# Kernel optimization log

Measured on AMD Instinct MI355X. Metric: run time of the kernel, lower is better.

Reference implementation:

```python
import jax, jax.numpy as jnp
import numpy as np

N = 100000
E = 1600000
D_IN = 50
D_H = 128
D_OUT = 128
EPS = 1e-5


def setup_inputs() -> dict:
    key = jax.random.key(0)
    ks = jax.random.split(key, 24)
    def w(k, shape, fan_in):
        return jax.random.normal(k, shape, jnp.float32) / np.sqrt(fan_in)
    inp = {
        'x': jax.random.normal(ks[0], (N, D_IN), jnp.float32),
        'edge_src': jax.random.randint(ks[1], (E,), 0, N, jnp.int32),
        'edge_dst': jax.random.randint(ks[2], (E,), 0, N, jnp.int32),
        # SAGEConv 1: D_IN -> D_H
        'Wl1': w(ks[3], (D_IN, D_H), D_IN), 'Wr1': w(ks[4], (D_IN, D_H), D_IN), 'b1': jnp.zeros((D_H,), jnp.float32),
        # SAGEConv 2: D_H -> D_H
        'Wl2': w(ks[5], (D_H, D_H), D_H), 'Wr2': w(ks[6], (D_H, D_H), D_H), 'b2': jnp.zeros((D_H,), jnp.float32),
        # SAGEConv 3: D_H -> D_OUT
        'Wl3': w(ks[7], (D_H, D_OUT), D_H), 'Wr3': w(ks[8], (D_H, D_OUT), D_H), 'b3': jnp.zeros((D_OUT,), jnp.float32),
        # skip linears (no bias)
        'Ws1': w(ks[9], (D_IN, D_H), D_IN), 'Ws2': w(ks[10], (D_IN, D_H), D_IN),
        # LayerNorm affine
        'lnw1': jnp.ones((D_H,), jnp.float32), 'lnb1': jnp.zeros((D_H,), jnp.float32),
        'lnw2': jnp.ones((D_H,), jnp.float32), 'lnb2': jnp.zeros((D_H,), jnp.float32),
        'lnw3': jnp.ones((D_OUT,), jnp.float32), 'lnb3': jnp.zeros((D_OUT,), jnp.float32),
        # PReLU scalar slopes (PyG init 0.25)
        'a1': jnp.float32(0.25), 'a2': jnp.float32(0.25), 'a3': jnp.float32(0.25),
    }
    return inp


def _sage(x, src, dst, Wl, Wr, b):
    # mean aggregation of source features at destinations, then linear + root
    msg = x[src]                                              # [E, d]
    agg = jax.ops.segment_sum(msg, dst, num_segments=N)       # [N, d]
    cnt = jax.ops.segment_sum(jnp.ones((src.shape[0],), x.dtype), dst, num_segments=N)
    mean = agg / jnp.maximum(cnt, 1.0)[:, None]
    return mean @ Wl + x @ Wr + b


def _graph_ln(x, w, b):
    # PyG LayerNorm mode='graph', batch=None: normalize over all nodes+channels
    xc = x - jnp.mean(x)
    std = jnp.sqrt(jnp.mean(xc * xc))
    return (xc / (std + EPS)) * w + b


def _prelu(x, a):
    return jnp.where(x >= 0, x, a * x)


def reference(x, edge_src, edge_dst, Wl1, Wr1, b1, Wl2, Wr2, b2, Wl3, Wr3, b3,
              Ws1, Ws2, lnw1, lnb1, lnw2, lnb2, lnw3, lnb3, a1, a2, a3):
    h1 = _sage(x, edge_src, edge_dst, Wl1, Wr1, b1)
    h1 = _prelu(_graph_ln(h1, lnw1, lnb1), a1)
    h2 = _sage(h1 + x @ Ws1, edge_src, edge_dst, Wl2, Wr2, b2)
    h2 = _prelu(_graph_ln(h2, lnw2, lnb2), a2)
    ret = _sage(h1 + h2 + x @ Ws2, edge_src, edge_dst, Wl3, Wr3, b3)
    ret = _prelu(_graph_ln(ret, lnw3, lnb3), a3)
    return ret
```

## Files before the change

### kernel.cpp

```cpp
#include <hip/hip_runtime.h>

#define D_IN 50
#define LN_EPS 1e-5f
#define BSH 8
#define MAXB 512
#define NSLOT 64

typedef __bf16 bf16_t;
typedef bf16_t bf16x8 __attribute__((ext_vector_type(8)));
typedef float f32x4_t __attribute__((ext_vector_type(4)));
typedef float f32x2_t __attribute__((ext_vector_type(2)));

#define STRIDE_ST 136

#define ACCP(r, A)                                                            \
    {                                                                         \
        A[0] += (f32x2_t){__uint_as_float((r).x << 16),                       \
                          __uint_as_float((r).x & 0xffff0000u)};              \
        A[1] += (f32x2_t){__uint_as_float((r).y << 16),                       \
                          __uint_as_float((r).y & 0xffff0000u)};              \
        A[2] += (f32x2_t){__uint_as_float((r).z << 16),                       \
                          __uint_as_float((r).z & 0xffff0000u)};              \
        A[3] += (f32x2_t){__uint_as_float((r).w << 16),                       \
                          __uint_as_float((r).w & 0xffff0000u)};              \
    }

__global__ void bucket_hist_k(const int* __restrict__ dst, int* __restrict__ bcnt,
                              double* __restrict__ lnacc, int e, int nb) {
    __shared__ int lh[MAXB];
    int t = threadIdx.x;
    if (blockIdx.x == 0 && t < 3 * NSLOT) {
        lnacc[t * 8] = 0.0;
        lnacc[t * 8 + 1] = 0.0;
    }
    for (int i = t; i < nb; i += 256) lh[i] = 0;
    __syncthreads();
    for (int i = blockIdx.x * 256 + t; i < e; i += gridDim.x * 256)
        atomicAdd(&lh[dst[i] >> BSH], 1);
    __syncthreads();
    for (int i = t; i < nb; i += 256) {
        int c = lh[i];
        if (c) atomicAdd(&bcnt[i * 16], c);
    }
}

__global__ void bscan_k(const int* __restrict__ bcnt, int* __restrict__ boff,
                        int* __restrict__ bpos, int nb, int e) {
    __shared__ int l[MAXB];
    int t = threadIdx.x;
    l[t] = (t < nb) ? bcnt[t * 16] : 0;
    __syncthreads();
    for (int off = 1; off < MAXB; off <<= 1) {
        int v = (t >= off) ? l[t - off] : 0;
        __syncthreads();
        l[t] += v;
        __syncthreads();
    }
    int excl = (t > 0) ? l[t - 1] : 0;
    if (t < nb) { boff[t] = excl; bpos[t * 16] = excl; }
    if (t == 0) boff[nb] = e;
}

__global__ void scatter_k(const int* __restrict__ src, const int* __restrict__ dst,
                          int* __restrict__ bpos, unsigned* __restrict__ pool,
                          int e, int nb) {
    __shared__ int lh[MAXB];
    __shared__ int lcur[MAXB];
    int t = threadIdx.x;
    for (int i = t; i < nb; i += 256) lh[i] = 0;
    __syncthreads();
    int chunk = (e + gridDim.x - 1) / gridDim.x;
    int s = blockIdx.x * chunk;
    int en = min(e, s + chunk);
    for (int i = s + t; i < en; i += 256)
        atomicAdd(&lh[dst[i] >> BSH], 1);
    __syncthreads();
    for (int i = t; i < nb; i += 256) {
        int c = lh[i];
        lcur[i] = c ? atomicAdd(&bpos[i * 16], c) : 0;
    }
    __syncthreads();
    for (int i = s + t; i < en; i += 256) {
        int d = dst[i];
        int p = atomicAdd(&lcur[d >> BSH], 1);
        pool[p] = (unsigned)src[i] | ((unsigned)(d & 255) << 17);
    }
}

__global__ void nhist_cfill_k(const unsigned* __restrict__ pool, const int* __restrict__ boff,
                              int* __restrict__ rp, int* __restrict__ col, int n) {
    __shared__ int lc[256];
    __shared__ int ls[256];
    __shared__ int lpos[256];
    int b = blockIdx.x, t = threadIdx.x;
    lc[t] = 0;
    __syncthreads();
    int s = boff[b], e = boff[b + 1];
    for (int i = s + t; i < e; i += 256) atomicAdd(&lc[pool[i] >> 17], 1);
    __syncthreads();
    int v = lc[t];
    ls[t] = v;
    __syncthreads();
    for (int off = 1; off < 256; off <<= 1) {
        int x = (t >= off) ? ls[t - off] : 0;
        __syncthreads();
        ls[t] += x;
        __syncthreads();
    }
    int excl = ls[t] - v;
    int nd = (b << BSH) + t;
    if (nd < n) rp[nd] = s + excl;
    if (nd == n - 1) rp[n] = e;
    lpos[t] = s + excl;
    __syncthreads();
    for (int i = s + t; i < e; i += 256) {
        unsigned pk = pool[i];
        int slot = atomicAdd(&lpos[pk >> 17], 1);
        col[slot] = (int)(pk & 0x1FFFFu);
    }
}

struct ConvDesc { const float* w; bf16_t* o; int kin; int kpad; };
struct ConvArgs { ConvDesc d[8]; };

__global__ void conv_w_k(ConvArgs args) {
    ConvDesc d = args.d[blockIdx.y];
    int i = blockIdx.x * 256 + threadIdx.x;
    int tot = 128 * d.kpad;
    if (i >= tot) return;
    int n = i / d.kpad, k = i - n * d.kpad;
    float v = (k < d.kin) ? d.w[(size_t)k * 128 + n] : 0.f;
    d.o[i] = (bf16_t)v;
}

__global__ void conv_x_k(const float* __restrict__ x, bf16_t* __restrict__ xb, int n) {
    int i = blockIdx.x * 256 + threadIdx.x;
    if (i >= n * 64) return;
    int node = i >> 6, k = i & 63;
    xb[i] = (k < D_IN) ? (bf16_t)x[node * D_IN + k] : (bf16_t)0.f;
}

__global__ void agg_bf64_k(const bf16_t* __restrict__ feat, const int* __restrict__ rp,
                           const int* __restrict__ col, bf16_t* __restrict__ mean, int n) {
    int wid = (blockIdx.x * blockDim.x + threadIdx.x) >> 6;
    int lane = threadIdx.x & 63;
    if (wid >= n) return;
    int start = rp[wid], end = rp[wid + 1];
    int lc = lane & 7;
    int g = lane >> 3;
    f32x2_t accA[4], accB[4];
#pragma unroll
    for (int k = 0; k < 4; k++) { accA[k] = (f32x2_t){0.f, 0.f}; accB[k] = (f32x2_t){0.f, 0.f}; }
    int e = start + g;
    if (e + 8 < end) {
        int i0 = col[e], i1 = col[e + 8];
        for (; e + 24 < end; e += 16) {
            uint4 r0 = *(const uint4*)(feat + (size_t)i0 * 64 + lc * 8);
            uint4 r1 = *(const uint4*)(feat + (size_t)i1 * 64 + lc * 8);
            i0 = col[e + 16];
            i1 = col[e + 24];
            ACCP(r0, accA);
            ACCP(r1, accB);
        }
        uint4 r0 = *(const uint4*)(feat + (size_t)i0 * 64 + lc * 8);
        uint4 r1 = *(const uint4*)(feat + (size_t)i1 * 64 + lc * 8);
        ACCP(r0, accA);
        ACCP(r1, accB);
        e += 16;
    }
    for (; e < end; e += 8) {
        uint4 r0 = *(const uint4*)(feat + (size_t)col[e] * 64 + lc * 8);
        ACCP(r0, accA);
    }
#pragma unroll
    for (int k = 0; k < 4; k++) accA[k] += accB[k];
    float aL[4], aH[4];
#pragma unroll
    for (int k = 0; k < 4; k++) { aL[k] = accA[k].x; aH[k] = accA[k].y; }
#pragma unroll
    for (int off = 8; off < 64; off <<= 1) {
#pragma unroll
        for (int k = 0; k < 4; k++) {
            aL[k] += __shfl_xor(aL[k], off);
            aH[k] += __shfl_xor(aH[k], off);
        }
    }
    int c = end - start;
    float invc = 1.f / (float)(c > 0 ? c : 1);
    if (lane < 8) {
        bf16x8 o;
#pragma unroll
        for (int k = 0; k < 4; k++) {
            o[2 * k] = (bf16_t)(aL[k] * invc);
            o[2 * k + 1] = (bf16_t)(aH[k] * invc);
        }
        *(bf16x8*)(mean + (size_t)wid * 64 + lc * 8) = o;
    }
}

__global__ void agg_bf128_k(const bf16_t* __restrict__ feat, const int* __restrict__ rp,
                            const int* __restrict__ col, bf16_t* __restrict__ mean, int n) {
    int wid = (blockIdx.x * blockDim.x + threadIdx.x) >> 6;
    int lane = threadIdx.x & 63;
    if (wid >= n) return;
    int start = rp[wid], end = rp[wid + 1];
    int lc = lane & 15;
    int g = lane >> 4;
    const uint* fp = (const uint*)feat + lc * 4;
    f32x2_t accA[4], accB[4];
#pragma unroll
    for (int k = 0; k < 4; k++) { accA[k] = (f32x2_t){0.f, 0.f}; accB[k] = (f32x2_t){0.f, 0.f}; }
    int e = start + g;
    int ng = (e < end) ? (((end - 1 - e) >> 2) + 1) : 0;
    int it = 0;
    for (; it + 4 <= ng; it += 4, e += 16) {
        int a = col[e], b = col[e + 4], c = col[e + 8], d = col[e + 12];
        uint4 r0 = *(const uint4*)(fp + (size_t)a * 64);
        uint4 r1 = *(const uint4*)(fp + (size_t)b * 64);
        uint4 r2 = *(const uint4*)(fp + (size_t)c * 64);
        uint4 r3 = *(const uint4*)(fp + (size_t)d * 64);
        ACCP(r0, accA);
        ACCP(r1, accB);
        ACCP(r2, accA);
        ACCP(r3, accB);
    }
    int rem = ng - it;
    if (rem > 0) {
        int a = col[e];
        int b = (rem > 1) ? col[e + 4] : a;
        int c = (rem > 2) ? col[e + 8] : b;
        uint4 r0 = *(const uint4*)(fp + (size_t)a * 64);
        uint4 r1 = *(const uint4*)(fp + (size_t)b * 64);
        uint4 r2 = *(const uint4*)(fp + (size_t)c * 64);
        ACCP(r0, accA);
        if (rem > 1) ACCP(r1, accB);
        if (rem > 2) ACCP(r2, accA);
    }
#pragma unroll
    for (int k = 0; k < 4; k++) accA[k] += accB[k];
    float aL[4], aH[4];
#pragma unroll
    for (int k = 0; k < 4; k++) { aL[k] = accA[k].x; aH[k] = accA[k].y; }
#pragma unroll
    for (int off = 16; off < 64; off <<= 1) {
#pragma unroll
        for (int k = 0; k < 4; k++) {
            aL[k] += __shfl_xor(aL[k], off);
            aH[k] += __shfl_xor(aH[k], off);
        }
    }
    int c = end - start;
    float invc = 1.f / (float)(c > 0 ? c : 1);
    if (lane < 16) {
        bf16x8 o;
#pragma unroll
        for (int k = 0; k < 4; k++) {
            o[2 * k] = (bf16_t)(aL[k] * invc);
            o[2 * k + 1] = (bf16_t)(aH[k] * invc);
        }
        *(bf16x8*)(mean + (size_t)wid * 128 + lc * 8) = o;
    }
}

template <int KPAD, bool DUAL>
__global__ __launch_bounds__(256) void mfma_gemm_k(
    const bf16_t* __restrict__ A, const bf16_t* __restrict__ B,
    const bf16_t* __restrict__ WlT, const bf16_t* __restrict__ WrT,
    const float* __restrict__ bias,
    bf16_t* __restrict__ out, double* __restrict__ lnacc, int M) {
    constexpr int KC = KPAD / 32;
    constexpr int WELE = 8 * KC * 64 * 8;
    __shared__ bf16_t lwl[WELE];
    __shared__ bf16_t lwr[DUAL ? WELE : 8];
    __shared__ float rsum[4], rsum2[4];

    const int tid = threadIdx.x;
    for (int ch = tid; ch < 8 * KC * 64; ch += 256) {
        int nt = ch / (KC * 64);
        int rem = ch - nt * (KC * 64);
        int c = rem >> 6;
        int ln = rem & 63;
        int mm = ln & 15, qq = ln >> 4;
        size_t srcoff = (size_t)(nt * 16 + mm) * KPAD + c * 32 + qq * 8;
        *(bf16x8*)&lwl[ch * 8] = *(const bf16x8*)(WlT + srcoff);
        if (DUAL) *(bf16x8*)&lwr[ch * 8] = *(const bf16x8*)(WrT + srcoff);
    }
    __syncthreads();

    const int w = tid >> 6;
    const int wid = blockIdx.x * 4 + w;
    const int lane = tid & 63;
    const int row0 = wid * 32;
    const int m = lane & 15;
    const int q = lane >> 4;
    const bool act = row0 < M;

    float lsum = 0.f, lsum2 = 0.f;
    if (act) {
        bf16x8 af[2][KC], bfr[DUAL ? 2 : 1][DUAL ? KC : 1];
#pragma unroll
        for (int s = 0; s < 2; s++) {
            const bf16_t* ar = A + (size_t)(row0 + s * 16 + m) * KPAD + q * 8;
#pragma unroll
            for (int c = 0; c < KC; c++) af[s][c] = *(const bf16x8*)(ar + c * 32);
            if (DUAL) {
                const bf16_t* br = B + (size_t)(row0 + s * 16 + m) * KPAD + q * 8;
#pragma unroll
                for (int c = 0; c < KC; c++) bfr[s][c] = *(const bf16x8*)(br + c * 32);
            }
        }
#pragma unroll
        for (int nt = 0; nt < 8; nt++) {
            f32x4_t acc0 = {0.f, 0.f, 0.f, 0.f};
            f32x4_t acc1 = {0.f, 0.f, 0.f, 0.f};
#pragma unroll
            for (int c = 0; c < KC; c++) {
                bf16x8 wv = *(const bf16x8*)&lwl[((nt * KC + c) * 64 + lane) * 8];
                acc0 = __builtin_amdgcn_mfma_f32_16x16x32_bf16(af[0][c], wv, acc0, 0, 0, 0);
                acc1 = __builtin_amdgcn_mfma_f32_16x16x32_bf16(af[1][c], wv, acc1, 0, 0, 0);
            }
            if (DUAL) {
#pragma unroll
                for (int c = 0; c < KC; c++) {
                    bf16x8 wv = *(const bf16x8*)&lwr[((nt * KC + c) * 64 + lane) * 8];
                    acc0 = __builtin_amdgcn_mfma_f32_16x16x32_bf16(bfr[0][c], wv, acc0, 0, 0, 0);
                    acc1 = __builtin_amdgcn_mfma_f32_16x16x32_bf16(bfr[1][c], wv, acc1, 0, 0, 0);
                }
            }
            float bv = bias ? bias[nt * 16 + m] : 0.f;
#pragma unroll
            for (int s = 0; s < 2; s++) {
                f32x4_t* ap = (s == 0) ? &acc0 : &acc1;
#pragma unroll
                for (int r = 0; r < 4; r++) {
                    int row = row0 + s * 16 + q * 4 + r;
                    if (row < M) {
                        float o = (*ap)[r] + bv;
                        out[(size_t)row * 128 + nt * 16 + m] = (bf16_t)o;
                        lsum += o; lsum2 += o * o;
                    }
                }
            }
        }
    }
    for (int off = 32; off > 0; off >>= 1) {
        lsum += __shfl_down(lsum, off);
        lsum2 += __shfl_down(lsum2, off);
    }
    if (lane == 0) { rsum[w] = lsum; rsum2[w] = lsum2; }
    __syncthreads();
    if (tid == 0) {
        double s = (double)rsum[0] + (double)rsum[1] + (double)rsum[2] + (double)rsum[3];
        double s2 = (double)rsum2[0] + (double)rsum2[1] + (double)rsum2[2] + (double)rsum2[3];
        int slot = (blockIdx.x & (NSLOT - 1)) * 8;
        unsafeAtomicAdd(&lnacc[slot], s);
        unsafeAtomicAdd(&lnacc[slot + 1], s2);
    }
}

__global__ __launch_bounds__(256) void mfma_gemm3_k(
    const bf16_t* __restrict__ A, const bf16_t* __restrict__ B,
    const bf16_t* __restrict__ WlT, const bf16_t* __restrict__ WrT,
    const bf16_t* __restrict__ Ws1T, const bf16_t* __restrict__ Ws2T,
    const float* __restrict__ bias,
    bf16_t* __restrict__ outP, bf16_t* __restrict__ outC1, bf16_t* __restrict__ outC2,
    double* __restrict__ lnacc, int M) {
    constexpr int KC = 2;
    constexpr int WELE = 8 * KC * 64 * 8;
    __shared__ bf16_t lwl[WELE];
    __shared__ bf16_t lwr[WELE];
    __shared__ __align__(16) bf16_t lst[4][16 * STRIDE_ST];
    __shared__ float rsum[4], rsum2[4];

    const int tid = threadIdx.x;
    for (int ch = tid; ch < 8 * KC * 64; ch += 256) {
        int nt = ch / (KC * 64);
        int rem = ch - nt * (KC * 64);
        int c = rem >> 6;
        int ln = rem & 63;
        int mm = ln & 15, qq = ln >> 4;
        size_t srcoff = (size_t)(nt * 16 + mm) * 64 + c * 32 + qq * 8;
        *(bf16x8*)&lwl[ch * 8] = *(const bf16x8*)(WlT + srcoff);
        *(bf16x8*)&lwr[ch * 8] = *(const bf16x8*)(WrT + srcoff);
    }
    __syncthreads();

    const int w = tid >> 6;
    const int wid = blockIdx.x * 4 + w;
    const int lane = tid & 63;
    const int row0 = wid * 32;
    const int m = lane & 15;
    const int q = lane >> 4;
    const bool act = row0 < M;

    float lsum = 0.f, lsum2 = 0.f;
    if (act) {
        bf16x8 af[2][KC], bfr[2][KC];
#pragma unroll
        for (int s = 0; s < 2; s++) {
            const bf16_t* ar = A + (size_t)(row0 + s * 16 + m) * 64 + q * 8;
            const bf16_t* br = B + (size_t)(row0 + s * 16 + m) * 64 + q * 8;
#pragma unroll
            for (int c = 0; c < KC; c++) {
                af[s][c] = *(const bf16x8*)(ar + c * 32);
                bfr[s][c] = *(const bf16x8*)(br + c * 32);
            }
        }
        bf16_t* st = lst[w];

#pragma unroll
        for (int s = 0; s < 2; s++) {
#pragma unroll
            for (int nt = 0; nt < 8; nt++) {
                f32x4_t acc = {0.f, 0.f, 0.f, 0.f};
#pragma unroll
                for (int c = 0; c < KC; c++) {
                    int wi = ((nt * KC + c) * 64 + lane) * 8;
                    bf16x8 wl = *(const bf16x8*)&lwl[wi];
                    bf16x8 wr = *(const bf16x8*)&lwr[wi];
                    acc = __builtin_amdgcn_mfma_f32_16x16x32_bf16(af[s][c], wl, acc, 0, 0, 0);
                    acc = __builtin_amdgcn_mfma_f32_16x16x32_bf16(bfr[s][c], wr, acc, 0, 0, 0);
                }
                float bv = bias[nt * 16 + m];
#pragma unroll
                for (int r = 0; r < 4; r++) {
                    float o = acc[r] + bv;
                    int row = row0 + s * 16 + q * 4 + r;
                    if (row < M) { lsum += o; lsum2 += o * o; }
                    st[(q * 4 + r) * STRIDE_ST + nt * 16 + m] = (bf16_t)o;
                }
            }
            int rowbase = row0 + s * 16;
#pragma unroll
            for (int k = 0; k < 4; k++) {
                int chunk = k * 64 + lane;
                int rr = chunk >> 4;
                int co = (chunk & 15) * 8;
                int row = rowbase + rr;
                bf16x8 v = *(bf16x8*)&st[rr * STRIDE_ST + co];
                if (row < M) *(bf16x8*)(outP + (size_t)row * 128 + co) = v;
            }
        }

#pragma unroll
        for (int p = 0; p < 2; p++) {
            const bf16_t* WT = (p == 0) ? Ws1T : Ws2T;
            bf16_t* outC = (p == 0) ? outC1 : outC2;
#pragma unroll
            for (int s = 0; s < 2; s++) {
#pragma unroll
                for (int nt = 0; nt < 8; nt++) {
                    f32x4_t acc = {0.f, 0.f, 0.f, 0.f};
#pragma unroll
                    for (int c = 0; c < KC; c++) {
                        size_t woff = (size_t)(nt * 16 + m) * 64 + c * 32 + q * 8;
                        bf16x8 wv = *(const bf16x8*)(WT + woff);
                        acc = __builtin_amdgcn_mfma_f32_16x16x32_bf16(bfr[s][c], wv, acc, 0, 0, 0);
                    }
#pragma unroll
                    for (int r = 0; r < 4; r++)
                        st[(q * 4 + r) * STRIDE_ST + nt * 16 + m] = (bf16_t)acc[r];
                }
                int rowbase = row0 + s * 16;
#pragma unroll
                for (int k = 0; k < 4; k++) {
                    int chunk = k * 64 + lane;
                    int rr = chunk >> 4;
                    int co = (chunk & 15) * 8;
                    int row = rowbase + rr;
                    bf16x8 v = *(bf16x8*)&st[rr * STRIDE_ST + co];
                    if (row < M) *(bf16x8*)(outC + (size_t)row * 128 + co) = v;
                }
            }
        }
    }
    for (int off = 32; off > 0; off >>= 1) {
        lsum += __shfl_down(lsum, off);
        lsum2 += __shfl_down(lsum2, off);
    }
    if (lane == 0) { rsum[w] = lsum; rsum2[w] = lsum2; }
    __syncthreads();
    if (tid == 0) {
        double s = (double)rsum[0] + (double)rsum[1] + (double)rsum[2] + (double)rsum[3];
        double s2 = (double)rsum2[0] + (double)rsum2[1] + (double)rsum2[2] + (double)rsum2[3];
        int slot = (blockIdx.x & (NSLOT - 1)) * 8;
        unsafeAtomicAdd(&lnacc[slot], s);
        unsafeAtomicAdd(&lnacc[slot + 1], s2);
    }
}

template <int MODE>
__global__ void ln_prelu_k(const bf16_t* __restrict__ pre, const bf16_t* __restrict__ h1in,
                           const bf16_t* __restrict__ s,
                           const float* __restrict__ lnw, const float* __restrict__ lnb,
                           const float* __restrict__ a_ptr, const double* __restrict__ acc,
                           void* __restrict__ out0v, void* __restrict__ out1v, int total) {
    __shared__ double ssum, ssum2;
    int t = threadIdx.x;
    if (t < 64) {
        double a = acc[t * 8];
        double b = acc[t * 8 + 1];
        for (int off = 32; off > 0; off >>= 1) {
            a += __shfl_down(a, off);
            b += __shfl_down(b, off);
        }
        if (t == 0) { ssum = a; ssum2 = b; }
    }
    __syncthreads();
    int i = blockIdx.x * blockDim.x + t;
    if (i * 8 >= total) return;
    double cinv = 1.0 / (double)total;
    double mm = ssum * cinv;
    double var = ssum2 * cinv - mm * mm;
    float stdv = (float)sqrt(var > 0.0 ? var : 0.0);
    float scale = 1.0f / (stdv + LN_EPS);
    float mf = (float)mm;
    float a = a_ptr[0];
    int c8 = i & 15;
    float4 w0 = ((const float4*)lnw)[c8 * 2];
    float4 w1 = ((const float4*)lnw)[c8 * 2 + 1];
    float4 b0 = ((const float4*)lnb)[c8 * 2];
    float4 b1 = ((const float4*)lnb)[c8 * 2 + 1];
    float wv[8] = {w0.x, w0.y, w0.z, w0.w, w1.x, w1.y, w1.z, w1.w};
    float bv[8] = {b0.x, b0.y, b0.z, b0.w, b1.x, b1.y, b1.z, b1.w};
    bf16x8 p8 = ((const bf16x8*)pre)[i];
    float h[8];
#pragma unroll
    for (int k = 0; k < 8; k++) {
        float v = ((float)p8[k] - mf) * scale * wv[k] + bv[k];
        h[k] = v >= 0.f ? v : a * v;
    }
    if (MODE == 1) {
        bf16x8 hb, tb;
        bf16x8 sv = ((const bf16x8*)s)[i];
#pragma unroll
        for (int k = 0; k < 8; k++) {
            hb[k] = (bf16_t)h[k];
            tb[k] = (bf16_t)(h[k] + (float)sv[k]);
        }
        ((bf16x8*)out0v)[i] = hb;
        ((bf16x8*)out1v)[i] = tb;
    } else if (MODE == 2) {
        bf16x8 hv = ((const bf16x8*)h1in)[i];
        bf16x8 sv = ((const bf16x8*)s)[i];
        bf16x8 tb;
#pragma unroll
        for (int k = 0; k < 8; k++)
            tb[k] = (bf16_t)((float)hv[k] + h[k] + (float)sv[k]);
        ((bf16x8*)out0v)[i] = tb;
    } else {
        float4 o0 = {h[0], h[1], h[2], h[3]};
        float4 o1 = {h[4], h[5], h[6], h[7]};
        ((float4*)out0v)[i * 2] = o0;
        ((float4*)out0v)[i * 2 + 1] = o1;
    }
}

extern "C" void kernel_launch(void* const* d_in, const int* in_sizes, int n_in,
                              void* d_out, int out_size, void* d_ws, size_t ws_size,
                              hipStream_t stream) {
    const float* x    = (const float*)d_in[0];
    const int*   esrc = (const int*)d_in[1];
    const int*   edst = (const int*)d_in[2];
    const float* Wl1  = (const float*)d_in[3];
    const float* Wr1  = (const float*)d_in[4];
    const float* b1   = (const float*)d_in[5];
    const float* Wl2  = (const float*)d_in[6];
    const float* Wr2  = (const float*)d_in[7];
    const float* b2   = (const float*)d_in[8];
    const float* Wl3  = (const float*)d_in[9];
    const float* Wr3  = (const float*)d_in[10];
    const float* b3   = (const float*)d_in[11];
    const float* Ws1  = (const float*)d_in[12];
    const float* Ws2  = (const float*)d_in[13];
    const float* lnw1 = (const float*)d_in[14];
    const float* lnb1 = (const float*)d_in[15];
    const float* lnw2 = (const float*)d_in[16];
    const float* lnb2 = (const float*)d_in[17];
    const float* lnw3 = (const float*)d_in[18];
    const float* lnb3 = (const float*)d_in[19];
    const float* a1   = (const float*)d_in[20];
    const float* a2   = (const float*)d_in[21];
    const float* a3   = (const float*)d_in[22];

    const int N = in_sizes[0] / D_IN;
    const int E = in_sizes[1];
    const int NB = (N + 255) >> BSH;

    char* ws = (char*)d_ws;
    size_t off = 0;
    auto alloc = [&](size_t bytes) -> void* {
        void* p = ws + off;
        off += (bytes + 255) & ~(size_t)255;
        return p;
    };
    bf16_t* xb   = (bf16_t*)alloc((size_t)N * 64 * 2);
    bf16_t* mean = (bf16_t*)alloc((size_t)N * 128 * 2);
    bf16_t* PRE  = (bf16_t*)alloc((size_t)N * 128 * 2);
    bf16_t* C1   = (bf16_t*)alloc((size_t)N * 128 * 2);
    bf16_t* C2   = (bf16_t*)alloc((size_t)N * 128 * 2);
    bf16_t* h1b  = (bf16_t*)alloc((size_t)N * 128 * 2);
    bf16_t* TB   = (bf16_t*)alloc((size_t)N * 128 * 2);
    bf16_t* WT   = (bf16_t*)alloc((size_t)(4 * 128 * 64 + 4 * 128 * 128) * 2);
    int* rp   = (int*)alloc((size_t)(N + 1) * 4);
    int* col  = (int*)alloc((size_t)E * 4);
    int* bcnt = (int*)alloc((size_t)MAXB * 16 * 4);
    int* boff = (int*)alloc((size_t)(MAXB + 1) * 4);
    int* bpos = (int*)alloc((size_t)MAXB * 16 * 4);
    unsigned* pool = (unsigned*)alloc((size_t)E * 4);
    double* lnacc = (double*)alloc((size_t)3 * NSLOT * 8 * 8);

    bf16_t* Wl1T = WT;
    bf16_t* Wr1T = Wl1T + 128 * 64;
    bf16_t* Ws1T = Wr1T + 128 * 64;
    bf16_t* Ws2T = Ws1T + 128 * 64;
    bf16_t* Wl2T = Ws2T + 128 * 64;
    bf16_t* Wr2T = Wl2T + 128 * 128;
    bf16_t* Wl3T = Wr2T + 128 * 128;
    bf16_t* Wr3T = Wl3T + 128 * 128;

    hipMemsetAsync(bcnt, 0, (size_t)MAXB * 16 * 4, stream);

    bucket_hist_k<<<256, 256, 0, stream>>>(edst, bcnt, lnacc, E, NB);
    bscan_k<<<1, MAXB, 0, stream>>>(bcnt, boff, bpos, NB, E);
    scatter_k<<<256, 256, 0, stream>>>(esrc, edst, bpos, pool, E, NB);
    nhist_cfill_k<<<NB, 256, 0, stream>>>(pool, boff, rp, col, N);

    ConvArgs ca;
    ca.d[0] = {Wl1, Wl1T, 50, 64};
    ca.d[1] = {Wr1, Wr1T, 50, 64};
    ca.d[2] = {Ws1, Ws1T, 50, 64};
    ca.d[3] = {Ws2, Ws2T, 50, 64};
    ca.d[4] = {Wl2, Wl2T, 128, 128};
    ca.d[5] = {Wr2, Wr2T, 128, 128};
    ca.d[6] = {Wl3, Wl3T, 128, 128};
    ca.d[7] = {Wr3, Wr3T, 128, 128};
    conv_w_k<<<dim3(64, 8), 256, 0, stream>>>(ca);
    conv_x_k<<<(N * 64 + 255) / 256, 256, 0, stream>>>(x, xb, N);

    const int aggBlocks = ((N * 64) + 255) / 256;
    const int tiles = (N + 31) / 32;
    const int gemmBlocks = (tiles + 3) / 4;
    const int lnBlocks = (N * 128 / 8 + 255) / 256;
    const int total = N * 128;
    double* acc1 = lnacc;
    double* acc2 = lnacc + NSLOT * 8;
    double* acc3 = lnacc + 2 * NSLOT * 8;

    agg_bf64_k<<<aggBlocks, 256, 0, stream>>>(xb, rp, col, mean, N);
    mfma_gemm3_k<<<gemmBlocks, 256, 0, stream>>>(
        mean, xb, Wl1T, Wr1T, Ws1T, Ws2T, b1, PRE, C1, C2, acc1, N);
    ln_prelu_k<1><<<lnBlocks, 256, 0, stream>>>(
        PRE, nullptr, C1, lnw1, lnb1, a1, acc1, h1b, TB, total);

    agg_bf128_k<<<aggBlocks, 256, 0, stream>>>(TB, rp, col, mean, N);
    mfma_gemm_k<128, true><<<gemmBlocks, 256, 0, stream>>>(
        mean, TB, Wl2T, Wr2T, b2, PRE, acc2, N);
    ln_prelu_k<2><<<lnBlocks, 256, 0, stream>>>(
        PRE, h1b, C2, lnw2, lnb2, a2, acc2, TB, nullptr, total);

    agg_bf128_k<<<aggBlocks, 256, 0, stream>>>(TB, rp, col, mean, N);
    mfma_gemm_k<128, true><<<gemmBlocks, 256, 0, stream>>>(
        mean, TB, Wl3T, Wr3T, b3, PRE, acc3, N);
    ln_prelu_k<3><<<lnBlocks, 256, 0, stream>>>(
        PRE, nullptr, nullptr, lnw3, lnb3, a3, acc3, d_out, nullptr, total);
}
```

Before: 521.1 us.

## Drop LDS weight staging and use 16-row strips with direct global weight loads

Both MFMA GEMM kernels stop staging the transposed weights in shared memory and read the MFMA B fragments straight from global memory (L1/L2 cached), which removes the per-block staging loop and its barrier. Each wave now handles a 16-row strip instead of 32 rows, doubling the block count, and the layer-1 kernel computes the root, skip-1 and skip-2 outputs together in one n-tile loop. Outputs are written as scalar bf16 stores instead of going through an LDS transpose buffer for vector stores. In exchange, weight reads are repeated per wave from cache, and the uncoalesced 2-byte stores may increase write traffic.

```diff
diff --git a/kernel.cpp b/kernel.cpp
--- a/kernel.cpp
+++ b/kernel.cpp
@@ -10,8 +10,6 @@
 typedef bf16_t bf16x8 __attribute__((ext_vector_type(8)));
 typedef float f32x4_t __attribute__((ext_vector_type(4)));
 typedef float f32x2_t __attribute__((ext_vector_type(2)));
-
-#define STRIDE_ST 136
 
 #define ACCP(r, A)                                                            \
     {                                                                         \
@@ -269,76 +267,55 @@
     const float* __restrict__ bias,
     bf16_t* __restrict__ out, double* __restrict__ lnacc, int M) {
     constexpr int KC = KPAD / 32;
-    constexpr int WELE = 8 * KC * 64 * 8;
-    __shared__ bf16_t lwl[WELE];
-    __shared__ bf16_t lwr[DUAL ? WELE : 8];
     __shared__ float rsum[4], rsum2[4];
 
     const int tid = threadIdx.x;
-    for (int ch = tid; ch < 8 * KC * 64; ch += 256) {
-        int nt = ch / (KC * 64);
-        int rem = ch - nt * (KC * 64);
-        int c = rem >> 6;
-        int ln = rem & 63;
-        int mm = ln & 15, qq = ln >> 4;
-        size_t srcoff = (size_t)(nt * 16 + mm) * KPAD + c * 32 + qq * 8;
-        *(bf16x8*)&lwl[ch * 8] = *(const bf16x8*)(WlT + srcoff);
-        if (DUAL) *(bf16x8*)&lwr[ch * 8] = *(const bf16x8*)(WrT + srcoff);
-    }
-    __syncthreads();
-
     const int w = tid >> 6;
     const int wid = blockIdx.x * 4 + w;
     const int lane = tid & 63;
-    const int row0 = wid * 32;
+    const int row0 = wid * 16;
     const int m = lane & 15;
     const int q = lane >> 4;
     const bool act = row0 < M;
 
     float lsum = 0.f, lsum2 = 0.f;
     if (act) {
-        bf16x8 af[2][KC], bfr[DUAL ? 2 : 1][DUAL ? KC : 1];
-#pragma unroll
-        for (int s = 0; s < 2; s++) {
-            const bf16_t* ar = A + (size_t)(row0 + s * 16 + m) * KPAD + q * 8;
-#pragma unroll
-            for (int c = 0; c < KC; c++) af[s][c] = *(const bf16x8*)(ar + c * 32);
+        bf16x8 af[KC], bfr[DUAL ? KC : 1];
+        {
+            const bf16_t* ar = A + (size_t)(row0 + m) * KPAD + q * 8;
+#pragma unroll
+            for (int c = 0; c < KC; c++) af[c] = *(const bf16x8*)(ar + c * 32);
             if (DUAL) {
-                const bf16_t* br = B + (size_t)(row0 + s * 16 + m) * KPAD + q * 8;
-#pragma unroll
-                for (int c = 0; c < KC; c++) bfr[s][c] = *(const bf16x8*)(br + c * 32);
+                const bf16_t* br = B + (size_t)(row0 + m) * KPAD + q * 8;
+#pragma unroll
+                for (int c = 0; c < KC; c++) bfr[c] = *(const bf16x8*)(br + c * 32);
             }
         }
 #pragma unroll
         for (int nt = 0; nt < 8; nt++) {
-            f32x4_t acc0 = {0.f, 0.f, 0.f, 0.f};
-            f32x4_t acc1 = {0.f, 0.f, 0.f, 0.f};
+            f32x4_t acc = {0.f, 0.f, 0.f, 0.f};
+            const bf16_t* wb1 = WlT + (size_t)(nt * 16 + m) * KPAD + q * 8;
+            const bf16_t* wb2 = WrT + (size_t)(nt * 16 + m) * KPAD + q * 8;
 #pragma unroll
             for (int c = 0; c < KC; c++) {
-                bf16x8 wv = *(const bf16x8*)&lwl[((nt * KC + c) * 64 + lane) * 8];
-                acc0 = __builtin_amdgcn_mfma_f32_16x16x32_bf16(af[0][c], wv, acc0, 0, 0, 0);
-                acc1 = __builtin_amdgcn_mfma_f32_16x16x32_bf16(af[1][c], wv, acc1, 0, 0, 0);
+                bf16x8 wl = *(const bf16x8*)(wb1 + c * 32);
+                acc = __builtin_amdgcn_mfma_f32_16x16x32_bf16(af[c], wl, acc, 0, 0, 0);
             }
             if (DUAL) {
 #pragma unroll
                 for (int c = 0; c < KC; c++) {
-                    bf16x8 wv = *(const bf16x8*)&lwr[((nt * KC + c) * 64 + lane) * 8];
-                    acc0 = __builtin_amdgcn_mfma_f32_16x16x32_bf16(bfr[0][c], wv, acc0, 0, 0, 0);
-                    acc1 = __builtin_amdgcn_mfma_f32_16x16x32_bf16(bfr[1][c], wv, acc1, 0, 0, 0);
+                    bf16x8 wr = *(const bf16x8*)(wb2 + c * 32);
+                    acc = __builtin_amdgcn_mfma_f32_16x16x32_bf16(bfr[c], wr, acc, 0, 0, 0);
                 }
             }
             float bv = bias ? bias[nt * 16 + m] : 0.f;
 #pragma unroll
-            for (int s = 0; s < 2; s++) {
-                f32x4_t* ap = (s == 0) ? &acc0 : &acc1;
-#pragma unroll
-                for (int r = 0; r < 4; r++) {
-                    int row = row0 + s * 16 + q * 4 + r;
-                    if (row < M) {
-                        float o = (*ap)[r] + bv;
-                        out[(size_t)row * 128 + nt * 16 + m] = (bf16_t)o;
-                        lsum += o; lsum2 += o * o;
-                    }
+            for (int r = 0; r < 4; r++) {
+                int row = row0 + q * 4 + r;
+                if (row < M) {
+                    float o = acc[r] + bv;
+                    out[(size_t)row * 128 + nt * 16 + m] = (bf16_t)o;
+                    lsum += o; lsum2 += o * o;
                 }
             }
         }
@@ -366,110 +343,57 @@
     bf16_t* __restrict__ outP, bf16_t* __restrict__ outC1, bf16_t* __restrict__ outC2,
     double* __restrict__ lnacc, int M) {
     constexpr int KC = 2;
-    constexpr int WELE = 8 * KC * 64 * 8;
-    __shared__ bf16_t lwl[WELE];
-    __shared__ bf16_t lwr[WELE];
-    __shared__ __align__(16) bf16_t lst[4][16 * STRIDE_ST];
     __shared__ float rsum[4], rsum2[4];
 
     const int tid = threadIdx.x;
-    for (int ch = tid; ch < 8 * KC * 64; ch += 256) {
-        int nt = ch / (KC * 64);
-        int rem = ch - nt * (KC * 64);
-        int c = rem >> 6;
-        int ln = rem & 63;
-        int mm = ln & 15, qq = ln >> 4;
-        size_t srcoff = (size_t)(nt * 16 + mm) * 64 + c * 32 + qq * 8;
-        *(bf16x8*)&lwl[ch * 8] = *(const bf16x8*)(WlT + srcoff);
-        *(bf16x8*)&lwr[ch * 8] = *(const bf16x8*)(WrT + srcoff);
-    }
-    __syncthreads();
-
     const int w = tid >> 6;
     const int wid = blockIdx.x * 4 + w;
     const int lane = tid & 63;
-    const int row0 = wid * 32;
+    const int row0 = wid * 16;
     const int m = lane & 15;
     const int q = lane >> 4;
     const bool act = row0 < M;
 
     float lsum = 0.f, lsum2 = 0.f;
     if (act) {
-        bf16x8 af[2][KC], bfr[2][KC];
-#pragma unroll
-        for (int s = 0; s < 2; s++) {
-            const bf16_t* ar = A + (size_t)(row0 + s * 16 + m) * 64 + q * 8;
-            const bf16_t* br = B + (size_t)(row0 + s * 16 + m) * 64 + q * 8;
+        bf16x8 af[KC], bfr[KC];
+        {
+            const bf16_t* ar = A + (size_t)(row0 + m) * 64 + q * 8;
+            const bf16_t* br = B + (size_t)(row0 + m) * 64 + q * 8;
 #pragma unroll
             for (int c = 0; c < KC; c++) {
-                af[s][c] = *(const bf16x8*)(ar + c * 32);
-                bfr[s][c] = *(const bf16x8*)(br + c * 32);
-            }
-        }
-        bf16_t* st = lst[w];
-
-#pragma unroll
-        for (int s = 0; s < 2; s++) {
-#pragma unroll
-            for (int nt = 0; nt < 8; nt++) {
-                f32x4_t acc = {0.f, 0.f, 0.f, 0.f};
-#pragma unroll
-                for (int c = 0; c < KC; c++) {
-                    int wi = ((nt * KC + c) * 64 + lane) * 8;
-                    bf16x8 wl = *(const bf16x8*)&lwl[wi];
-                    bf16x8 wr = *(const bf16x8*)&lwr[wi];
-                    acc = __builtin_amdgcn_mfma_f32_16x16x32_bf16(af[s][c], wl, acc, 0, 0, 0);
-                    acc = __builtin_amdgcn_mfma_f32_16x16x32_bf16(bfr[s][c], wr, acc, 0, 0, 0);
-                }
-                float bv = bias[nt * 16 + m];
-#pragma unroll
-                for (int r = 0; r < 4; r++) {
-                    float o = acc[r] + bv;
-                    int row = row0 + s * 16 + q * 4 + r;
-                    if (row < M) { lsum += o; lsum2 += o * o; }
-                    st[(q * 4 + r) * STRIDE_ST + nt * 16 + m] = (bf16_t)o;
-                }
-            }
-            int rowbase = row0 + s * 16;
-#pragma unroll
-            for (int k = 0; k < 4; k++) {
-                int chunk = k * 64 + lane;
-                int rr = chunk >> 4;
-                int co = (chunk & 15) * 8;
-                int row = rowbase + rr;
-                bf16x8 v = *(bf16x8*)&st[rr * STRIDE_ST + co];
-                if (row < M) *(bf16x8*)(outP + (size_t)row * 128 + co) = v;
-            }
-        }
-
-#pragma unroll
-        for (int p = 0; p < 2; p++) {
-            const bf16_t* WT = (p == 0) ? Ws1T : Ws2T;
-            bf16_t* outC = (p == 0) ? outC1 : outC2;
-#pragma unroll
-            for (int s = 0; s < 2; s++) {
-#pragma unroll
-                for (int nt = 0; nt < 8; nt++) {
-                    f32x4_t acc = {0.f, 0.f, 0.f, 0.f};
-#pragma unroll
-                    for (int c = 0; c < KC; c++) {
-                        size_t woff = (size_t)(nt * 16 + m) * 64 + c * 32 + q * 8;
-                        bf16x8 wv = *(const bf16x8*)(WT + woff);
-                        acc = __builtin_amdgcn_mfma_f32_16x16x32_bf16(bfr[s][c], wv, acc, 0, 0, 0);
-                    }
-#pragma unroll
-                    for (int r = 0; r < 4; r++)
-                        st[(q * 4 + r) * STRIDE_ST + nt * 16 + m] = (bf16_t)acc[r];
-                }
-                int rowbase = row0 + s * 16;
-#pragma unroll
-                for (int k = 0; k < 4; k++) {
-                    int chunk = k * 64 + lane;
-                    int rr = chunk >> 4;
-                    int co = (chunk & 15) * 8;
-                    int row = rowbase + rr;
-                    bf16x8 v = *(bf16x8*)&st[rr * STRIDE_ST + co];
-                    if (row < M) *(bf16x8*)(outC + (size_t)row * 128 + co) = v;
+                af[c] = *(const bf16x8*)(ar + c * 32);
+                bfr[c] = *(const bf16x8*)(br + c * 32);
+            }
+        }
+#pragma unroll
+        for (int nt = 0; nt < 8; nt++) {
+            f32x4_t aP = {0.f, 0.f, 0.f, 0.f};
+            f32x4_t a1 = {0.f, 0.f, 0.f, 0.f};
+            f32x4_t a2 = {0.f, 0.f, 0.f, 0.f};
+            size_t wb = (size_t)(nt * 16 + m) * 64 + q * 8;
+#pragma unroll
+            for (int c = 0; c < KC; c++) {
+                bf16x8 wl = *(const bf16x8*)(WlT + wb + c * 32);
+                bf16x8 wr = *(const bf16x8*)(WrT + wb + c * 32);
+                bf16x8 w1 = *(const bf16x8*)(Ws1T + wb + c * 32);
+                bf16x8 w2 = *(const bf16x8*)(Ws2T + wb + c * 32);
+                aP = __builtin_amdgcn_mfma_f32_16x16x32_bf16(af[c], wl, aP, 0, 0, 0);
+                aP = __builtin_amdgcn_mfma_f32_16x16x32_bf16(bfr[c], wr, aP, 0, 0, 0);
+                a1 = __builtin_amdgcn_mfma_f32_16x16x32_bf16(bfr[c], w1, a1, 0, 0, 0);
+                a2 = __builtin_amdgcn_mfma_f32_16x16x32_bf16(bfr[c], w2, a2, 0, 0, 0);
+            }
+            float bv = bias[nt * 16 + m];
+#pragma unroll
+            for (int r = 0; r < 4; r++) {
+                int row = row0 + q * 4 + r;
+                if (row < M) {
+                    float o = aP[r] + bv;
+                    size_t oi = (size_t)row * 128 + nt * 16 + m;
+                    outP[oi] = (bf16_t)o;
+                    outC1[oi] = (bf16_t)a1[r];
+                    outC2[oi] = (bf16_t)a2[r];
+                    lsum += o; lsum2 += o * o;
                 }
             }
         }
@@ -639,8 +563,8 @@
     conv_x_k<<<(N * 64 + 255) / 256, 256, 0, stream>>>(x, xb, N);
 
     const int aggBlocks = ((N * 64) + 255) / 256;
-    const int tiles = (N + 31) / 32;
-    const int gemmBlocks = (tiles + 3) / 4;
+    const int strips = (N + 15) / 16;
+    const int gemmBlocks = (strips + 3) / 4;
     const int lnBlocks = (N * 128 / 8 + 255) / 256;
     const int total = N * 128;
     double* acc1 = lnacc;
```

Measured after the change: 592.8 us. 13.7% more time.
